# Performance work log

Measured on AMD Instinct MI355X. Metric: run time of the kernel, lower is better.

The kernel has to match this reference:

```python
import jax, jax.numpy as jnp
import numpy as np

B, S, D = 2, 2048, 1024
H, DK, DV = 16, 64, 64
N_WINDOW = 256
LN_EPS = 1e-5


def setup_inputs() -> dict:
    key = jax.random.key(0)
    ks = jax.random.split(key, 8)
    sc = 0.02
    return {
        "Q": jax.random.normal(ks[0], (B, S, D), jnp.float32),
        "K": jax.random.normal(ks[1], (B, S, D), jnp.float32),
        "V": jax.random.normal(ks[2], (B, S, D), jnp.float32),
        "Wq": jax.random.normal(ks[3], (D, H * DK), jnp.float32) * sc,
        "bq": jnp.zeros((H * DK,), jnp.float32),
        "Wk": jax.random.normal(ks[4], (D, H * DK), jnp.float32) * sc,
        "bk": jnp.zeros((H * DK,), jnp.float32),
        "Wv": jax.random.normal(ks[5], (D, H * DV), jnp.float32) * sc,
        "bv": jnp.zeros((H * DV,), jnp.float32),
        "Wo": jax.random.normal(ks[6], (H * DV, D), jnp.float32) * sc,
        "bo": jnp.zeros((D,), jnp.float32),
        "gamma": jnp.ones((D,), jnp.float32),
        "beta": jnp.zeros((D,), jnp.float32),
    }


def reference(Q, K, V, Wq, bq, Wk, bk, Wv, bv, Wo, bo, gamma, beta):
    b, s, _ = Q.shape
    # QKV projections -> [b, s, h, d]
    q = (Q @ Wq + bq).reshape(b, s, H, DK)
    k = (K @ Wk + bk).reshape(b, s, H, DK)
    v = (V @ Wv + bv).reshape(b, s, H, DV)
    # scores [b, h, i, j]
    scores = jnp.einsum("bihd,bjhd->bhij", q, k) / np.sqrt(DK).astype(np.float32)
    # sliding-window band mask |i - j| < N_WINDOW (mask=True path)
    idx = jnp.arange(s)
    band = jnp.abs(idx[:, None] - idx[None, :]) < N_WINDOW  # [s, s]
    scores = jnp.where(band[None, None], scores, -jnp.inf)
    attn = jax.nn.softmax(scores, axis=-1)
    ctx = jnp.einsum("bhij,bjhd->bihd", attn, v).reshape(b, s, H * DV)
    out = ctx @ Wo + bo
    # residual + LayerNorm over last dim
    x = out + Q
    mu = jnp.mean(x, axis=-1, keepdims=True)
    var = jnp.mean(jnp.square(x - mu), axis=-1, keepdims=True)
    y = (x - mu) * jax.lax.rsqrt(var + LN_EPS) * gamma + beta
    return y, attn
```

## Files before the change

### kernel.cpp

```cpp
#include <hip/hip_runtime.h>
#include <hip/hip_bf16.h>

#define BB 2
#define SS 2048
#define HH 16
#define LN_EPS 1e-5f
#define LOG2E 1.44269504088896f

typedef __attribute__((ext_vector_type(8))) short short8;
typedef __attribute__((ext_vector_type(4))) float floatx4;

#define EXP2F(x) __builtin_amdgcn_exp2f(x)
#define GLOAD16(g, l) __builtin_amdgcn_global_load_lds( \
    (const __attribute__((address_space(1))) void*)(g), \
    (__attribute__((address_space(3))) void*)(l), 16, 0, 0)

__device__ __forceinline__ ushort f2b(float f) {
    union { float f; unsigned u; } x; x.f = f;
    unsigned u = x.u;
    return (ushort)((u + 0x7FFFu + ((u >> 16) & 1u)) >> 16);
}
__device__ __forceinline__ float b2f(ushort u) {
    union { unsigned u; float f; } x; x.u = ((unsigned)u) << 16;
    return x.f;
}

__global__ __launch_bounds__(256) void to_bf16(
    const float* __restrict__ X0, const float* __restrict__ X1, const float* __restrict__ X2,
    ushort* __restrict__ Y0, ushort* __restrict__ Y1, ushort* __restrict__ Y2)
{
    const int z = blockIdx.z;
    const float* X = z == 0 ? X0 : z == 1 ? X1 : X2;
    ushort* Y = z == 0 ? Y0 : z == 1 ? Y1 : Y2;
    const size_t i = ((size_t)blockIdx.x * 256 + threadIdx.x) * 8;
    float4 a = *(const float4*)&X[i];
    float4 b = *(const float4*)&X[i + 4];
    short8 o;
    o[0] = (short)f2b(a.x); o[1] = (short)f2b(a.y); o[2] = (short)f2b(a.z); o[3] = (short)f2b(a.w);
    o[4] = (short)f2b(b.x); o[5] = (short)f2b(b.y); o[6] = (short)f2b(b.z); o[7] = (short)f2b(b.w);
    *(short8*)&Y[i] = o;
}

__global__ __launch_bounds__(256) void wtrans(
    const float* __restrict__ W0, const float* __restrict__ W1,
    const float* __restrict__ W2, const float* __restrict__ W3,
    ushort* __restrict__ T0, ushort* __restrict__ T1,
    ushort* __restrict__ T2, ushort* __restrict__ T3)
{
    const int z = blockIdx.z;
    const float* W = z == 0 ? W0 : z == 1 ? W1 : z == 2 ? W2 : W3;
    ushort* T = z == 0 ? T0 : z == 1 ? T1 : z == 2 ? T2 : T3;
    const float scale = (z == 0) ? 0.125f : 1.0f;
    __shared__ float ts[32][33];
    const int k0 = blockIdx.y * 32, n0 = blockIdx.x * 32;
    const int r = threadIdx.x >> 3, c4 = (threadIdx.x & 7) * 4;
    float4 v = *(const float4*)&W[(size_t)(k0 + r) * 1024 + n0 + c4];
    ts[r][c4 + 0] = v.x; ts[r][c4 + 1] = v.y; ts[r][c4 + 2] = v.z; ts[r][c4 + 3] = v.w;
    __syncthreads();
    ushort4 o;
    o.x = f2b(ts[c4 + 0][r] * scale); o.y = f2b(ts[c4 + 1][r] * scale);
    o.z = f2b(ts[c4 + 2][r] * scale); o.w = f2b(ts[c4 + 3][r] * scale);
    *(ushort4*)&T[(size_t)(n0 + r) * 1024 + k0 + c4] = o;
}

__device__ __forceinline__ void gemm_body(
    const ushort* __restrict__ Ab, const ushort* __restrict__ Bt,
    const float* __restrict__ bias, float bscale,
    float* Cf, ushort* Cb, int m0, int n0)
{
    __shared__ ushort As[2][128 * 32];
    __shared__ ushort Bs[2][128 * 32];
    const int t = threadIdx.x;
    const int l = t & 63;
    const int w = t >> 6;
    const int wm = w >> 1, wn = w & 1;

    floatx4 acc[4][4] = {};

    const int i0c = w * 64 + l;
    const int r0 = i0c >> 2, c0 = i0c & 3;
    const int i1c = 256 + i0c;
    const int r1 = i1c >> 2, c1 = i1c & 3;

    const ushort* gA0 = &Ab[(size_t)(m0 + r0) * 1024 + c0 * 8];
    const ushort* gA1 = &Ab[(size_t)(m0 + r1) * 1024 + c1 * 8];
    const ushort* gB0 = &Bt[(size_t)(n0 + r0) * 1024 + c0 * 8];
    const ushort* gB1 = &Bt[(size_t)(n0 + r1) * 1024 + c1 * 8];

    const int d0 = (w * 64) * 16;
    const int d1 = (256 + w * 64) * 16;

    GLOAD16(gA0, (char*)As[0] + d0);
    GLOAD16(gA1, (char*)As[0] + d1);
    GLOAD16(gB0, (char*)Bs[0] + d0);
    GLOAD16(gB1, (char*)Bs[0] + d1);
    __syncthreads();

    int cur = 0;
    for (int k0 = 0; k0 < 1024; k0 += 32) {
        if (k0 + 32 < 1024) {
            GLOAD16(gA0 + k0 + 32, (char*)As[cur ^ 1] + d0);
            GLOAD16(gA1 + k0 + 32, (char*)As[cur ^ 1] + d1);
            GLOAD16(gB0 + k0 + 32, (char*)Bs[cur ^ 1] + d0);
            GLOAD16(gB1 + k0 + 32, (char*)Bs[cur ^ 1] + d1);
        }
        short8 af[4], bf[4];
#pragma unroll
        for (int m = 0; m < 4; ++m)
            af[m] = *(const short8*)&As[cur][(wm * 64 + m * 16 + (l & 15)) * 32 + (l >> 4) * 8];
#pragma unroll
        for (int n = 0; n < 4; ++n)
            bf[n] = *(const short8*)&Bs[cur][(wn * 64 + n * 16 + (l & 15)) * 32 + (l >> 4) * 8];
#pragma unroll
        for (int m = 0; m < 4; ++m)
#pragma unroll
            for (int n = 0; n < 4; ++n)
                acc[m][n] = __builtin_amdgcn_mfma_f32_16x16x32_bf16(af[m], bf[n], acc[m][n], 0, 0, 0);
        __syncthreads();
        cur ^= 1;
    }

    const int cr = (l >> 4) * 4;
    const int cc = l & 15;
#pragma unroll
    for (int n = 0; n < 4; ++n) {
        int col = n0 + wn * 64 + n * 16 + cc;
        float bv = bias[col] * bscale;
#pragma unroll
        for (int m = 0; m < 4; ++m) {
            int row = m0 + wm * 64 + m * 16 + cr;
#pragma unroll
            for (int j = 0; j < 4; ++j) {
                float v = acc[m][n][j] + bv;
                if (Cf) Cf[(size_t)(row + j) * 1024 + col] = v;
                else    Cb[(size_t)(row + j) * 1024 + col] = f2b(v);
            }
        }
    }
}

__device__ __forceinline__ void swz_mn(int& m0, int& n0) {
    int bid = blockIdx.x + (blockIdx.y << 3);
    int xcd = bid & 7, idx = bid >> 3;
    m0 = (xcd * 4 + (idx & 3)) * 128;
    n0 = (idx >> 2) * 128;
}

__global__ __launch_bounds__(256) void gemm_qkv(
    const ushort* __restrict__ Xq, const ushort* __restrict__ Xk, const ushort* __restrict__ Xv,
    const ushort* __restrict__ Wqt, const ushort* __restrict__ Wkt, const ushort* __restrict__ Wvt,
    const float* __restrict__ bq, const float* __restrict__ bk, const float* __restrict__ bv,
    ushort* __restrict__ qp, ushort* __restrict__ kp, ushort* __restrict__ vp)
{
    const int z = blockIdx.z;
    const ushort* A = z == 0 ? Xq : z == 1 ? Xk : Xv;
    const ushort* Bt = z == 0 ? Wqt : z == 1 ? Wkt : Wvt;
    const float* bias = z == 0 ? bq : z == 1 ? bk : bv;
    ushort* C = z == 0 ? qp : z == 1 ? kp : vp;
    float bscale = (z == 0) ? 0.125f : 1.0f;
    int m0, n0; swz_mn(m0, n0);
    gemm_body(A, Bt, bias, bscale, nullptr, C, m0, n0);
}

__global__ __launch_bounds__(256) void gemm_obf(
    const ushort* __restrict__ ctxb, const ushort* __restrict__ Wot,
    const float* __restrict__ bo, float* __restrict__ op)
{
    int m0, n0; swz_mn(m0, n0);
    gemm_body(ctxb, Wot, bo, 1.0f, op, nullptr, m0, n0);
}

__global__ __launch_bounds__(256, 4) void attn_mfma(
    const ushort* __restrict__ qb, const ushort* __restrict__ kb, const ushort* __restrict__ vb,
    float* __restrict__ attn, ushort* __restrict__ ctxb)
{
    __shared__ alignas(16) ushort Vt[2][64 * 72];
    __shared__ alignas(16) ushort Pl[4][16 * 72];

    const int qblk = blockIdx.x, h = blockIdx.y, b = blockIdx.z;
    const int i0 = qblk * 64;
    const int t = threadIdx.x;
    const int w = t >> 6, l = t & 63;
    const int g = l >> 4, c = l & 15;
    const int ibase = i0 + w * 16;

    const int jstart = max(0, i0 - 256);
    const int jend = min(SS, i0 + 64 + 256);

    const size_t qoff = (size_t)(b * SS + ibase + c) * 1024 + h * 64 + g * 8;
    short8 aq0 = *(const short8*)&qb[qoff];
    short8 aq1 = *(const short8*)&qb[qoff + 32];

    const int vj0 = (t & 31) * 2, vd0 = (t >> 5) * 8;
    const ushort* Kbh = &kb[(size_t)(b * SS) * 1024 + h * 64];

    float m[4] = {-3e38f, -3e38f, -3e38f, -3e38f};
    float ll[4] = {0.f, 0.f, 0.f, 0.f};

    for (int jt = jstart; jt < jend; jt += 64) {
        const ushort* kt = Kbh + (size_t)jt * 1024;
        floatx4 s[4] = {};
#pragma unroll
        for (int u = 0; u < 4; ++u) {
            short8 b0 = *(const short8*)&kt[(size_t)(u * 16 + c) * 1024 + g * 8];
            short8 b1 = *(const short8*)&kt[(size_t)(u * 16 + c) * 1024 + 32 + g * 8];
            s[u] = __builtin_amdgcn_mfma_f32_16x16x32_bf16(aq0, b0, s[u], 0, 0, 0);
            s[u] = __builtin_amdgcn_mfma_f32_16x16x32_bf16(aq1, b1, s[u], 0, 0, 0);
        }
        const bool full = (jt >= ibase - 240) && (jt <= ibase + 192);
#pragma unroll
        for (int r = 0; r < 4; ++r) {
            float v0 = s[0][r] * LOG2E, v1 = s[1][r] * LOG2E,
                  v2 = s[2][r] * LOG2E, v3 = s[3][r] * LOG2E;
            if (!full) {
                const int i = ibase + g * 4 + r;
                const int j0 = jt + c;
                if ((unsigned)(i - j0 + 255) >= 511u)        v0 = -3e38f;
                if ((unsigned)(i - (j0 + 16) + 255) >= 511u) v1 = -3e38f;
                if ((unsigned)(i - (j0 + 32) + 255) >= 511u) v2 = -3e38f;
                if ((unsigned)(i - (j0 + 48) + 255) >= 511u) v3 = -3e38f;
            }
            float tmax = fmaxf(fmaxf(v0, v1), fmaxf(v2, v3));
            float mn = fmaxf(m[r], tmax);
            float sc_ = EXP2F(m[r] - mn);
            float add = EXP2F(v0 - mn) + EXP2F(v1 - mn)
                      + EXP2F(v2 - mn) + EXP2F(v3 - mn);
            ll[r] = ll[r] * sc_ + add;
            m[r] = mn;
        }
    }

    float M[4], invL[4];
#pragma unroll
    for (int r = 0; r < 4; ++r) {
        float mm = m[r];
        mm = fmaxf(mm, __shfl_xor(mm, 1));
        mm = fmaxf(mm, __shfl_xor(mm, 2));
        mm = fmaxf(mm, __shfl_xor(mm, 4));
        mm = fmaxf(mm, __shfl_xor(mm, 8));
        float la = ll[r] * EXP2F(m[r] - mm);
        la += __shfl_xor(la, 1);
        la += __shfl_xor(la, 2);
        la += __shfl_xor(la, 4);
        la += __shfl_xor(la, 8);
        M[r] = mm;
        invL[r] = 1.0f / la;
    }

    {
        const ushort* vr = &vb[(size_t)(b * SS + jstart + vj0) * 1024 + h * 64 + vd0];
        short8 v0 = *(const short8*)vr;
        short8 v1 = *(const short8*)(vr + 1024);
#pragma unroll
        for (int e = 0; e < 8; ++e) {
            ushort2 pr; pr.x = (ushort)v0[e]; pr.y = (ushort)v1[e];
            *(ushort2*)&Vt[0][(vd0 + e) * 72 + vj0] = pr;
        }
    }
    __syncthreads();

    floatx4 ctx[4] = {};
    int cur = 0;
    for (int jt = jstart; jt < jend; jt += 64) {
        const bool have = (jt + 64 < jend);
        short8 nv0, nv1;
        if (have) {
            const ushort* vr = &vb[(size_t)(b * SS + jt + 64 + vj0) * 1024 + h * 64 + vd0];
            nv0 = *(const short8*)vr;
            nv1 = *(const short8*)(vr + 1024);
        }
        const ushort* kt = Kbh + (size_t)jt * 1024;
        floatx4 s[4] = {};
#pragma unroll
        for (int u = 0; u < 4; ++u) {
            short8 b0 = *(const short8*)&kt[(size_t)(u * 16 + c) * 1024 + g * 8];
            short8 b1 = *(const short8*)&kt[(size_t)(u * 16 + c) * 1024 + 32 + g * 8];
            s[u] = __builtin_amdgcn_mfma_f32_16x16x32_bf16(aq0, b0, s[u], 0, 0, 0);
            s[u] = __builtin_amdgcn_mfma_f32_16x16x32_bf16(aq1, b1, s[u], 0, 0, 0);
        }
        const bool full = (jt >= ibase - 240) && (jt <= ibase + 192);
#pragma unroll
        for (int u = 0; u < 4; ++u) {
#pragma unroll
            for (int r = 0; r < 4; ++r) {
                float v = s[u][r] * LOG2E;
                if (!full) {
                    const int i = ibase + g * 4 + r;
                    const int j = jt + u * 16 + c;
                    if ((unsigned)(i - j + 255) >= 511u) v = -3e38f;
                }
                float p = EXP2F(v - M[r]) * invL[r];
                Pl[w][(g * 4 + r) * 72 + u * 16 + c] = f2b(p);
            }
        }
#pragma unroll
        for (int it = 0; it < 4; ++it) {
            const int row = it * 4 + g;
            ushort4 pw = *(const ushort4*)&Pl[w][row * 72 + c * 4];
            floatx4 o;
            o[0] = b2f(pw.x); o[1] = b2f(pw.y); o[2] = b2f(pw.z); o[3] = b2f(pw.w);
            __builtin_nontemporal_store(o,
                (floatx4*)&attn[(size_t)(b * HH + h) * SS * SS + (size_t)(ibase + row) * SS + jt + c * 4]);
        }
#pragma unroll
        for (int jc = 0; jc < 2; ++jc) {
            short8 pa = *(const short8*)&Pl[w][c * 72 + jc * 32 + g * 8];
#pragma unroll
            for (int ds = 0; ds < 4; ++ds) {
                short8 bv_ = *(const short8*)&Vt[cur][(ds * 16 + c) * 72 + jc * 32 + g * 8];
                ctx[ds] = __builtin_amdgcn_mfma_f32_16x16x32_bf16(pa, bv_, ctx[ds], 0, 0, 0);
            }
        }
        if (have) {
#pragma unroll
            for (int e = 0; e < 8; ++e) {
                ushort2 pr; pr.x = (ushort)nv0[e]; pr.y = (ushort)nv1[e];
                *(ushort2*)&Vt[cur ^ 1][(vd0 + e) * 72 + vj0] = pr;
            }
        }
        __syncthreads();
        cur ^= 1;
    }

#pragma unroll
    for (int ds = 0; ds < 4; ++ds)
#pragma unroll
        for (int r = 0; r < 4; ++r)
            ctxb[(size_t)(b * SS + ibase + g * 4 + r) * 1024 + h * 64 + ds * 16 + c] = f2b(ctx[ds][r]);

    {
        float* ab = attn + (size_t)(b * HH + h) * SS * SS;
        const floatx4 z4 = {0.f, 0.f, 0.f, 0.f};
        const int g16 = t >> 4, c16 = t & 15;
#pragma unroll
        for (int rr = 0; rr < 4; ++rr) {
            float* rp = ab + (size_t)(i0 + g16 + rr * 16) * SS;
            for (int x = c16 * 4; x < jstart; x += 64)
                __builtin_nontemporal_store(z4, (floatx4*)&rp[x]);
            for (int x = jend + c16 * 4; x < SS; x += 64)
                __builtin_nontemporal_store(z4, (floatx4*)&rp[x]);
        }
    }
}

__global__ __launch_bounds__(256) void ln_kernel(
    const float* __restrict__ op, const float* __restrict__ Qin,
    const float* __restrict__ gamma, const float* __restrict__ beta,
    float* __restrict__ y)
{
    const int row = blockIdx.x;
    const int t = threadIdx.x;
    __shared__ float rs[4], rss[4];

    float4 o4 = *(const float4*)&op[(size_t)row * 1024 + t * 4];
    float4 q4 = *(const float4*)&Qin[(size_t)row * 1024 + t * 4];
    float x0 = o4.x + q4.x, x1 = o4.y + q4.y, x2 = o4.z + q4.z, x3 = o4.w + q4.w;
    float s = x0 + x1 + x2 + x3;
    float ss = x0 * x0 + x1 * x1 + x2 * x2 + x3 * x3;
#pragma unroll
    for (int off = 1; off < 64; off <<= 1) {
        s  += __shfl_xor(s, off, 64);
        ss += __shfl_xor(ss, off, 64);
    }
    int wid = t >> 6;
    if ((t & 63) == 0) { rs[wid] = s; rss[wid] = ss; }
    __syncthreads();
    s  = rs[0] + rs[1] + rs[2] + rs[3];
    ss = rss[0] + rss[1] + rss[2] + rss[3];
    float mu = s * (1.0f / 1024.0f);
    float var = ss * (1.0f / 1024.0f) - mu * mu;
    float rstd = rsqrtf(var + LN_EPS);
    float4 g4 = *(const float4*)&gamma[t * 4];
    float4 b4 = *(const float4*)&beta[t * 4];
    float4 o;
    o.x = (x0 - mu) * rstd * g4.x + b4.x;
    o.y = (x1 - mu) * rstd * g4.y + b4.y;
    o.z = (x2 - mu) * rstd * g4.z + b4.z;
    o.w = (x3 - mu) * rstd * g4.w + b4.w;
    *(float4*)&y[(size_t)row * 1024 + t * 4] = o;
}

extern "C" void kernel_launch(void* const* d_in, const int* in_sizes, int n_in,
                              void* d_out, int out_size, void* d_ws, size_t ws_size,
                              hipStream_t stream) {
    (void)in_sizes; (void)n_in; (void)out_size; (void)ws_size;
    const float* Q  = (const float*)d_in[0];
    const float* K  = (const float*)d_in[1];
    const float* V  = (const float*)d_in[2];
    const float* Wq = (const float*)d_in[3];
    const float* bq = (const float*)d_in[4];
    const float* Wk = (const float*)d_in[5];
    const float* bk = (const float*)d_in[6];
    const float* Wv = (const float*)d_in[7];
    const float* bv = (const float*)d_in[8];
    const float* Wo = (const float*)d_in[9];
    const float* bo = (const float*)d_in[10];
    const float* gamma = (const float*)d_in[11];
    const float* beta  = (const float*)d_in[12];

    float* y = (float*)d_out;
    float* attn = y + (size_t)BB * SS * 1024;

    char* base = (char*)d_ws;
    float*  op   = (float*)base;
    ushort* Xq   = (ushort*)base;
    ushort* Xk   = (ushort*)(base + (size_t)8 * 1048576);
    ushort* Xv   = (ushort*)(base + (size_t)16 * 1048576);
    ushort* ctxb = (ushort*)(base + (size_t)16 * 1048576);
    ushort* qbp  = (ushort*)(base + (size_t)24 * 1048576);
    ushort* kbp  = (ushort*)(base + (size_t)32 * 1048576);
    ushort* vbp  = (ushort*)(base + (size_t)40 * 1048576);
    ushort* Wqt  = (ushort*)(base + (size_t)48 * 1048576);
    ushort* Wkt  = (ushort*)(base + (size_t)50 * 1048576);
    ushort* Wvt  = (ushort*)(base + (size_t)52 * 1048576);
    ushort* Wot  = (ushort*)(base + (size_t)54 * 1048576);

    to_bf16<<<dim3(2048, 1, 3), 256, 0, stream>>>(Q, K, V, Xq, Xk, Xv);
    wtrans<<<dim3(32, 32, 4), 256, 0, stream>>>(Wq, Wk, Wv, Wo, Wqt, Wkt, Wvt, Wot);
    gemm_qkv<<<dim3(8, 32, 3), 256, 0, stream>>>(Xq, Xk, Xv, Wqt, Wkt, Wvt, bq, bk, bv, qbp, kbp, vbp);
    attn_mfma<<<dim3(SS / 64, HH, BB), 256, 0, stream>>>(qbp, kbp, vbp, attn, ctxb);
    gemm_obf<<<dim3(8, 32), 256, 0, stream>>>(ctxb, Wot, bo, op);
    ln_kernel<<<4096, 256, 0, stream>>>(op, Q, gamma, beta, y);
}
```

Measured before the change: 236.6 us.

## Merge prep kernels, narrow output GEMM tile, issue attn zero-fill early

Merges the bf16 conversion and weight transpose into one prep launch to cut a kernel launch. Templates the GEMM body on N-tile width and runs the output projection with 128x64 tiles, doubling block count for better CU occupancy. Moves the out-of-band zero stores of the attention matrix to the start of the attention kernel so they can overlap with compute. The trade-off is less reuse per block in the output GEMM and more register pressure early in the attention kernel.

Measured after the change: 225.9 us, median of 2. -4.5%, faster.

```diff
diff --git a/kernel.cpp b/kernel.cpp
--- a/kernel.cpp
+++ b/kernel.cpp
@@ -25,57 +25,58 @@
     return x.f;
 }
 
-__global__ __launch_bounds__(256) void to_bf16(
-    const float* __restrict__ X0, const float* __restrict__ X1, const float* __restrict__ X2,
-    ushort* __restrict__ Y0, ushort* __restrict__ Y1, ushort* __restrict__ Y2)
-{
-    const int z = blockIdx.z;
-    const float* X = z == 0 ? X0 : z == 1 ? X1 : X2;
-    ushort* Y = z == 0 ? Y0 : z == 1 ? Y1 : Y2;
-    const size_t i = ((size_t)blockIdx.x * 256 + threadIdx.x) * 8;
-    float4 a = *(const float4*)&X[i];
-    float4 b = *(const float4*)&X[i + 4];
-    short8 o;
-    o[0] = (short)f2b(a.x); o[1] = (short)f2b(a.y); o[2] = (short)f2b(a.z); o[3] = (short)f2b(a.w);
-    o[4] = (short)f2b(b.x); o[5] = (short)f2b(b.y); o[6] = (short)f2b(b.z); o[7] = (short)f2b(b.w);
-    *(short8*)&Y[i] = o;
-}
-
-__global__ __launch_bounds__(256) void wtrans(
+__global__ __launch_bounds__(256) void prep(
+    const float* __restrict__ Q, const float* __restrict__ K, const float* __restrict__ V,
     const float* __restrict__ W0, const float* __restrict__ W1,
     const float* __restrict__ W2, const float* __restrict__ W3,
+    ushort* __restrict__ Xq, ushort* __restrict__ Xk, ushort* __restrict__ Xv,
     ushort* __restrict__ T0, ushort* __restrict__ T1,
     ushort* __restrict__ T2, ushort* __restrict__ T3)
 {
+    __shared__ float ts[32][33];
     const int z = blockIdx.z;
-    const float* W = z == 0 ? W0 : z == 1 ? W1 : z == 2 ? W2 : W3;
-    ushort* T = z == 0 ? T0 : z == 1 ? T1 : z == 2 ? T2 : T3;
-    const float scale = (z == 0) ? 0.125f : 1.0f;
-    __shared__ float ts[32][33];
-    const int k0 = blockIdx.y * 32, n0 = blockIdx.x * 32;
-    const int r = threadIdx.x >> 3, c4 = (threadIdx.x & 7) * 4;
-    float4 v = *(const float4*)&W[(size_t)(k0 + r) * 1024 + n0 + c4];
-    ts[r][c4 + 0] = v.x; ts[r][c4 + 1] = v.y; ts[r][c4 + 2] = v.z; ts[r][c4 + 3] = v.w;
-    __syncthreads();
-    ushort4 o;
-    o.x = f2b(ts[c4 + 0][r] * scale); o.y = f2b(ts[c4 + 1][r] * scale);
-    o.z = f2b(ts[c4 + 2][r] * scale); o.w = f2b(ts[c4 + 3][r] * scale);
-    *(ushort4*)&T[(size_t)(n0 + r) * 1024 + k0 + c4] = o;
-}
-
+    if (z < 3) {
+        const float* X = z == 0 ? Q : z == 1 ? K : V;
+        ushort* Y = z == 0 ? Xq : z == 1 ? Xk : Xv;
+        const size_t i = ((size_t)blockIdx.x * 256 + threadIdx.x) * 8;
+        float4 a = *(const float4*)&X[i];
+        float4 b = *(const float4*)&X[i + 4];
+        short8 o;
+        o[0] = (short)f2b(a.x); o[1] = (short)f2b(a.y); o[2] = (short)f2b(a.z); o[3] = (short)f2b(a.w);
+        o[4] = (short)f2b(b.x); o[5] = (short)f2b(b.y); o[6] = (short)f2b(b.z); o[7] = (short)f2b(b.w);
+        *(short8*)&Y[i] = o;
+    } else {
+        if (blockIdx.x >= 1024) return;
+        const int zz = z - 3;
+        const float* W = zz == 0 ? W0 : zz == 1 ? W1 : zz == 2 ? W2 : W3;
+        ushort* T = zz == 0 ? T0 : zz == 1 ? T1 : zz == 2 ? T2 : T3;
+        const float scale = (zz == 0) ? 0.125f : 1.0f;
+        const int k0 = (blockIdx.x >> 5) * 32, n0 = (blockIdx.x & 31) * 32;
+        const int r = threadIdx.x >> 3, c4 = (threadIdx.x & 7) * 4;
+        float4 v = *(const float4*)&W[(size_t)(k0 + r) * 1024 + n0 + c4];
+        ts[r][c4 + 0] = v.x; ts[r][c4 + 1] = v.y; ts[r][c4 + 2] = v.z; ts[r][c4 + 3] = v.w;
+        __syncthreads();
+        ushort4 o;
+        o.x = f2b(ts[c4 + 0][r] * scale); o.y = f2b(ts[c4 + 1][r] * scale);
+        o.z = f2b(ts[c4 + 2][r] * scale); o.w = f2b(ts[c4 + 3][r] * scale);
+        *(ushort4*)&T[(size_t)(n0 + r) * 1024 + k0 + c4] = o;
+    }
+}
+
+template<int NB>
 __device__ __forceinline__ void gemm_body(
     const ushort* __restrict__ Ab, const ushort* __restrict__ Bt,
     const float* __restrict__ bias, float bscale,
     float* Cf, ushort* Cb, int m0, int n0)
 {
     __shared__ ushort As[2][128 * 32];
-    __shared__ ushort Bs[2][128 * 32];
+    __shared__ ushort Bs[2][NB * 32 * 32];
     const int t = threadIdx.x;
     const int l = t & 63;
     const int w = t >> 6;
     const int wm = w >> 1, wn = w & 1;
 
-    floatx4 acc[4][4] = {};
+    floatx4 acc[4][NB] = {};
 
     const int i0c = w * 64 + l;
     const int r0 = i0c >> 2, c0 = i0c & 3;
@@ -85,7 +86,7 @@
     const ushort* gA0 = &Ab[(size_t)(m0 + r0) * 1024 + c0 * 8];
     const ushort* gA1 = &Ab[(size_t)(m0 + r1) * 1024 + c1 * 8];
     const ushort* gB0 = &Bt[(size_t)(n0 + r0) * 1024 + c0 * 8];
-    const ushort* gB1 = &Bt[(size_t)(n0 + r1) * 1024 + c1 * 8];
+    const ushort* gB1 = &Bt[(size_t)(n0 + ((NB == 4) ? r1 : r0)) * 1024 + ((NB == 4) ? c1 : c0) * 8];
 
     const int d0 = (w * 64) * 16;
     const int d1 = (256 + w * 64) * 16;
@@ -93,7 +94,7 @@
     GLOAD16(gA0, (char*)As[0] + d0);
     GLOAD16(gA1, (char*)As[0] + d1);
     GLOAD16(gB0, (char*)Bs[0] + d0);
-    GLOAD16(gB1, (char*)Bs[0] + d1);
+    if (NB == 4) GLOAD16(gB1, (char*)Bs[0] + d1);
     __syncthreads();
 
     int cur = 0;
@@ -102,19 +103,19 @@
             GLOAD16(gA0 + k0 + 32, (char*)As[cur ^ 1] + d0);
             GLOAD16(gA1 + k0 + 32, (char*)As[cur ^ 1] + d1);
             GLOAD16(gB0 + k0 + 32, (char*)Bs[cur ^ 1] + d0);
-            GLOAD16(gB1 + k0 + 32, (char*)Bs[cur ^ 1] + d1);
-        }
-        short8 af[4], bf[4];
+            if (NB == 4) GLOAD16(gB1 + k0 + 32, (char*)Bs[cur ^ 1] + d1);
+        }
+        short8 af[4], bf[NB];
 #pragma unroll
         for (int m = 0; m < 4; ++m)
             af[m] = *(const short8*)&As[cur][(wm * 64 + m * 16 + (l & 15)) * 32 + (l >> 4) * 8];
 #pragma unroll
-        for (int n = 0; n < 4; ++n)
-            bf[n] = *(const short8*)&Bs[cur][(wn * 64 + n * 16 + (l & 15)) * 32 + (l >> 4) * 8];
+        for (int n = 0; n < NB; ++n)
+            bf[n] = *(const short8*)&Bs[cur][(wn * (NB * 16) + n * 16 + (l & 15)) * 32 + (l >> 4) * 8];
 #pragma unroll
         for (int m = 0; m < 4; ++m)
 #pragma unroll
-            for (int n = 0; n < 4; ++n)
+            for (int n = 0; n < NB; ++n)
                 acc[m][n] = __builtin_amdgcn_mfma_f32_16x16x32_bf16(af[m], bf[n], acc[m][n], 0, 0, 0);
         __syncthreads();
         cur ^= 1;
@@ -123,8 +124,8 @@
     const int cr = (l >> 4) * 4;
     const int cc = l & 15;
 #pragma unroll
-    for (int n = 0; n < 4; ++n) {
-        int col = n0 + wn * 64 + n * 16 + cc;
+    for (int n = 0; n < NB; ++n) {
+        int col = n0 + wn * (NB * 16) + n * 16 + cc;
         float bv = bias[col] * bscale;
 #pragma unroll
         for (int m = 0; m < 4; ++m) {
@@ -137,13 +138,6 @@
             }
         }
     }
-}
-
-__device__ __forceinline__ void swz_mn(int& m0, int& n0) {
-    int bid = blockIdx.x + (blockIdx.y << 3);
-    int xcd = bid & 7, idx = bid >> 3;
-    m0 = (xcd * 4 + (idx & 3)) * 128;
-    n0 = (idx >> 2) * 128;
 }
 
 __global__ __launch_bounds__(256) void gemm_qkv(
@@ -158,16 +152,22 @@
     const float* bias = z == 0 ? bq : z == 1 ? bk : bv;
     ushort* C = z == 0 ? qp : z == 1 ? kp : vp;
     float bscale = (z == 0) ? 0.125f : 1.0f;
-    int m0, n0; swz_mn(m0, n0);
-    gemm_body(A, Bt, bias, bscale, nullptr, C, m0, n0);
+    int bid = blockIdx.x + (blockIdx.y << 3);
+    int xcd = bid & 7, idx = bid >> 3;
+    int m0 = (xcd * 4 + (idx & 3)) * 128;
+    int n0 = (idx >> 2) * 128;
+    gemm_body<4>(A, Bt, bias, bscale, nullptr, C, m0, n0);
 }
 
 __global__ __launch_bounds__(256) void gemm_obf(
     const ushort* __restrict__ ctxb, const ushort* __restrict__ Wot,
     const float* __restrict__ bo, float* __restrict__ op)
 {
-    int m0, n0; swz_mn(m0, n0);
-    gemm_body(ctxb, Wot, bo, 1.0f, op, nullptr, m0, n0);
+    int bid = blockIdx.x + (blockIdx.y << 3);
+    int xcd = bid & 7, idx = bid >> 3;
+    int m0 = (xcd * 4 + (idx & 3)) * 128;
+    int n0 = (idx >> 2) * 64;
+    gemm_body<2>(ctxb, Wot, bo, 1.0f, op, nullptr, m0, n0);
 }
 
 __global__ __launch_bounds__(256, 4) void attn_mfma(
@@ -190,6 +190,20 @@
     const size_t qoff = (size_t)(b * SS + ibase + c) * 1024 + h * 64 + g * 8;
     short8 aq0 = *(const short8*)&qb[qoff];
     short8 aq1 = *(const short8*)&qb[qoff + 32];
+
+    {
+        float* ab = attn + (size_t)(b * HH + h) * SS * SS;
+        const floatx4 z4 = {0.f, 0.f, 0.f, 0.f};
+        const int g16 = t >> 4, c16 = t & 15;
+#pragma unroll
+        for (int rr = 0; rr < 4; ++rr) {
+            float* rp = ab + (size_t)(i0 + g16 + rr * 16) * SS;
+            for (int x = c16 * 4; x < jstart; x += 64)
+                __builtin_nontemporal_store(z4, (floatx4*)&rp[x]);
+            for (int x = jend + c16 * 4; x < SS; x += 64)
+                __builtin_nontemporal_store(z4, (floatx4*)&rp[x]);
+        }
+    }
 
     const int vj0 = (t & 31) * 2, vd0 = (t >> 5) * 8;
     const ushort* Kbh = &kb[(size_t)(b * SS) * 1024 + h * 64];
@@ -327,20 +341,6 @@
 #pragma unroll
         for (int r = 0; r < 4; ++r)
             ctxb[(size_t)(b * SS + ibase + g * 4 + r) * 1024 + h * 64 + ds * 16 + c] = f2b(ctx[ds][r]);
-
-    {
-        float* ab = attn + (size_t)(b * HH + h) * SS * SS;
-        const floatx4 z4 = {0.f, 0.f, 0.f, 0.f};
-        const int g16 = t >> 4, c16 = t & 15;
-#pragma unroll
-        for (int rr = 0; rr < 4; ++rr) {
-            float* rp = ab + (size_t)(i0 + g16 + rr * 16) * SS;
-            for (int x = c16 * 4; x < jstart; x += 64)
-                __builtin_nontemporal_store(z4, (floatx4*)&rp[x]);
-            for (int x = jend + c16 * 4; x < SS; x += 64)
-                __builtin_nontemporal_store(z4, (floatx4*)&rp[x]);
-        }
-    }
 }
 
 __global__ __launch_bounds__(256) void ln_kernel(
@@ -415,10 +415,10 @@
     ushort* Wvt  = (ushort*)(base + (size_t)52 * 1048576);
     ushort* Wot  = (ushort*)(base + (size_t)54 * 1048576);
 
-    to_bf16<<<dim3(2048, 1, 3), 256, 0, stream>>>(Q, K, V, Xq, Xk, Xv);
-    wtrans<<<dim3(32, 32, 4), 256, 0, stream>>>(Wq, Wk, Wv, Wo, Wqt, Wkt, Wvt, Wot);
+    prep<<<dim3(2048, 1, 7), 256, 0, stream>>>(Q, K, V, Wq, Wk, Wv, Wo,
+                                               Xq, Xk, Xv, Wqt, Wkt, Wvt, Wot);
     gemm_qkv<<<dim3(8, 32, 3), 256, 0, stream>>>(Xq, Xk, Xv, Wqt, Wkt, Wvt, bq, bk, bv, qbp, kbp, vbp);
     attn_mfma<<<dim3(SS / 64, HH, BB), 256, 0, stream>>>(qbp, kbp, vbp, attn, ctxb);
-    gemm_obf<<<dim3(8, 32), 256, 0, stream>>>(ctxb, Wot, bo, op);
+    gemm_obf<<<dim3(8, 64), 256, 0, stream>>>(ctxb, Wot, bo, op);
     ln_kernel<<<4096, 256, 0, stream>>>(op, Q, gamma, beta, y);
 }
```
